# Optimization experiments

Hardware: AMD Instinct MI355X
Metric: run time of the kernel (lower is better)

The kernel has to match this reference:

```python
import jax, jax.numpy as jnp
import numpy as np

B, NN, F, H = 8, 1024, 256, 8
D = F // H
SCALE = D ** -0.5


def setup_inputs() -> dict:
    key = jax.random.key(0)
    ks = jax.random.split(key, 12)
    s = 0.02
    inp = {
        'ndata': jax.random.normal(ks[0], (B, NN, F), jnp.float32),
        'N': NN,
        'attn_bias': jax.random.normal(ks[1], (B, NN, NN, H), jnp.float32),
        'attn_mask': jax.random.randint(ks[2], (B, NN, NN), 0, 2).astype(bool),
        'Wq': jax.random.normal(ks[3], (F, F), jnp.float32) * s,
        'bq': jnp.zeros((F,), jnp.float32),
        'Wk': jax.random.normal(ks[4], (F, F), jnp.float32) * s,
        'bk': jnp.zeros((F,), jnp.float32),
        'Wv': jax.random.normal(ks[5], (F, F), jnp.float32) * s,
        'bv': jnp.zeros((F,), jnp.float32),
        'Wo': jax.random.normal(ks[6], (F, F), jnp.float32) * s,
        'bo': jnp.zeros((F,), jnp.float32),
    }
    return inp


def reference(ndata, N, attn_bias, attn_mask, Wq, bq, Wk, bk, Wv, bv, Wo, bo):
    b, n, f = ndata.shape
    # QKV projections (torch nn.Linear: x @ W.T + b), split heads
    q = (ndata @ Wq.T + bq).reshape(b, n, H, D) * SCALE
    k = (ndata @ Wk.T + bk).reshape(b, n, H, D)
    v = (ndata @ Wv.T + bv).reshape(b, n, H, D)
    # scores: (b, q, k, h) matching torch layout after its transposes
    scores = jnp.einsum('bqhd,bkhd->bqkh', q, k)
    scores = scores + attn_bias  # additive bias
    # original code force-unmasks column 0 so every row has a valid entry
    mask = attn_mask.at[:, :, 0].set(False)
    scores = jnp.where(mask[..., None], -jnp.inf, scores)
    attn = jax.nn.softmax(scores, axis=2)  # softmax over keys
    out = jnp.einsum('bqkh,bkhd->bqhd', attn, v).reshape(b, n, f)
    return out @ Wo.T + bo
```

## Files before the change

kernel.cpp:

```cpp
#include <hip/hip_runtime.h>
#include <hip/hip_bf16.h>

typedef __attribute__((ext_vector_type(8))) short short8;
typedef __attribute__((ext_vector_type(4))) float f32x4;

#define MFMA16(a,b,c) __builtin_amdgcn_mfma_f32_16x16x32_bf16((a),(b),(c),0,0,0)

static __device__ __forceinline__ unsigned int f2bf(float f){
    unsigned int u = __float_as_uint(f);
    u += 0x7FFFu + ((u >> 16) & 1u);
    return u >> 16;
}

static __device__ __forceinline__ short8 pack8(float4 a, float4 b){
    short8 r;
    r[0]=(short)f2bf(a.x); r[1]=(short)f2bf(a.y);
    r[2]=(short)f2bf(a.z); r[3]=(short)f2bf(a.w);
    r[4]=(short)f2bf(b.x); r[5]=(short)f2bf(b.y);
    r[6]=(short)f2bf(b.z); r[7]=(short)f2bf(b.w);
    return r;
}

__global__ __launch_bounds__(256) void mask_prep_k(
    const unsigned int* __restrict__ m, unsigned int* __restrict__ bmout)
{
    __shared__ int any_hi;
    const int tid  = threadIdx.x;
    const int lane = tid & 63;
    const unsigned int gbase = blockIdx.x*256u + tid;
    if (tid == 0) any_hi = 0;

    unsigned int wv[8]; unsigned int acc = 0;
    #pragma unroll
    for (int it = 0; it < 8; ++it){
        wv[it] = m[it*262144u + gbase];
        acc |= wv[it];
    }
    __syncthreads();
    if (acc & 0xFFFFFF00u) atomicOr(&any_hi, 1);
    __syncthreads();

    if (any_hi == 0){
        for (int it = 0; it < 32; ++it){
            unsigned int idx = it*262144u + gbase;
            unsigned int v = m[idx];
            unsigned long long bal = __ballot(v != 0u);
            if (lane == 0)
                *(unsigned long long*)(bmout + (idx >> 5)) = bal;
        }
    } else {
        #pragma unroll
        for (int it = 0; it < 8; ++it){
            unsigned int idx = it*262144u + gbase;
            unsigned int v = wv[it];
            unsigned int nib = (v | (v>>7) | (v>>14) | (v>>21)) & 0xFu;
            unsigned int x = nib << ((lane & 7)*4);
            x |= (unsigned int)__shfl_xor((int)x, 1);
            x |= (unsigned int)__shfl_xor((int)x, 2);
            x |= (unsigned int)__shfl_xor((int)x, 4);
            if ((lane & 7) == 0)
                bmout[idx >> 3] = x;
        }
    }
}

__global__ __launch_bounds__(256) void qkv_proj_k(
    const float* __restrict__ nd,
    const float* __restrict__ Wqp, const float* __restrict__ bqp,
    const float* __restrict__ Wkp, const float* __restrict__ bkp,
    const float* __restrict__ Wvp, const float* __restrict__ bvp,
    unsigned short* __restrict__ qout, unsigned short* __restrict__ kout,
    unsigned short* __restrict__ vtout)
{
    __shared__ __align__(16) unsigned short xl[64*264];
    const int tid  = threadIdx.x;
    const int bi   = blockIdx.x;
    const int kind = bi >> 7;
    const int R0   = (bi & 127) * 64;
    const int b    = R0 >> 10;
    const int n0   = R0 & 1023;

    #pragma unroll
    for (int it = 0; it < 16; ++it){
        int f4 = it*256 + tid;
        int r = f4 >> 6, c4 = f4 & 63;
        float4 v = *(const float4*)(nd + (size_t)(R0+r)*256 + c4*4);
        unsigned int lo = f2bf(v.x) | (f2bf(v.y) << 16);
        unsigned int hi = f2bf(v.z) | (f2bf(v.w) << 16);
        *(uint2*)&xl[r*264 + c4*4] = make_uint2(lo, hi);
    }
    __syncthreads();

    const int lane = tid & 63;
    const int w  = tid >> 6;
    const int ln = lane & 15;
    const int g  = lane >> 4;
    const int ow = w * 64;

    f32x4 acc[4][4];
    #pragma unroll
    for (int a=0;a<4;++a){
        #pragma unroll
        for (int c=0;c<4;++c) acc[a][c] = (f32x4){0.f,0.f,0.f,0.f};
    }

    if (kind < 2){
        const float* W  = kind ? Wkp : Wqp;
        const float* bb = kind ? bkp : bqp;
        unsigned short* op = kind ? kout : qout;
        const float scl = kind ? 1.0f : 0.17677669529663687f;
        for (int kk = 0; kk < 8; ++kk){
            short8 wf[4], xf[4];
            #pragma unroll
            for (int ot=0; ot<4; ++ot){
                const float* wp = W + (size_t)(ow + ot*16 + ln)*256 + kk*32 + g*8;
                wf[ot] = pack8(*(const float4*)wp, *(const float4*)(wp+4));
            }
            #pragma unroll
            for (int nt=0; nt<4; ++nt)
                xf[nt] = *(const short8*)&xl[(nt*16+ln)*264 + kk*32 + g*8];
            #pragma unroll
            for (int ot=0; ot<4; ++ot){
                #pragma unroll
                for (int nt=0; nt<4; ++nt)
                    acc[ot][nt] = MFMA16(wf[ot], xf[nt], acc[ot][nt]);
            }
        }
        #pragma unroll
        for (int ot=0; ot<4; ++ot){
            int o0 = ow + ot*16 + g*4;
            int h = o0 >> 5, d0 = o0 & 31;
            float4 b4 = *(const float4*)(bb + o0);
            #pragma unroll
            for (int nt=0; nt<4; ++nt){
                int n = n0 + nt*16 + ln;
                unsigned int lo = f2bf((acc[ot][nt][0]+b4.x)*scl) | (f2bf((acc[ot][nt][1]+b4.y)*scl)<<16);
                unsigned int hi = f2bf((acc[ot][nt][2]+b4.z)*scl) | (f2bf((acc[ot][nt][3]+b4.w)*scl)<<16);
                *(uint2*)(op + ((size_t)(b*8+h)*1024 + n)*32 + d0) = make_uint2(lo,hi);
            }
        }
    } else {
        for (int kk = 0; kk < 8; ++kk){
            short8 wf[4], xf[4];
            #pragma unroll
            for (int ot=0; ot<4; ++ot){
                const float* wp = Wvp + (size_t)(ow + ot*16 + ln)*256 + kk*32 + g*8;
                wf[ot] = pack8(*(const float4*)wp, *(const float4*)(wp+4));
            }
            #pragma unroll
            for (int nt=0; nt<4; ++nt)
                xf[nt] = *(const short8*)&xl[(nt*16+ln)*264 + kk*32 + g*8];
            #pragma unroll
            for (int nt=0; nt<4; ++nt){
                #pragma unroll
                for (int ot=0; ot<4; ++ot)
                    acc[nt][ot] = MFMA16(xf[nt], wf[ot], acc[nt][ot]);
            }
        }
        #pragma unroll
        for (int nt=0; nt<4; ++nt){
            int nb = n0 + nt*16 + g*4;
            #pragma unroll
            for (int ot=0; ot<4; ++ot){
                int o = ow + ot*16 + ln;
                int h = o >> 5, d = o & 31;
                float bvv = bvp[o];
                unsigned int lo = f2bf(acc[nt][ot][0]+bvv) | (f2bf(acc[nt][ot][1]+bvv)<<16);
                unsigned int hi = f2bf(acc[nt][ot][2]+bvv) | (f2bf(acc[nt][ot][3]+bvv)<<16);
                *(uint2*)(vtout + ((size_t)(b*8+h)*32 + d)*1024 + nb) = make_uint2(lo,hi);
            }
        }
    }
}

__global__ __launch_bounds__(512, 4) void attn_k(
    const unsigned short* __restrict__ qbuf, const unsigned short* __restrict__ kbuf,
    const unsigned short* __restrict__ vtbuf, const float* __restrict__ bias,
    const unsigned int* __restrict__ bm, unsigned short* __restrict__ ab)
{
    __shared__ __align__(16) float bs[8704];
    const int tid  = threadIdx.x;
    const int bi   = blockIdx.x;
    const int b    = bi >> 6;
    const int q0   = (bi & 63) * 16;
    const int lane = tid & 63;
    const int w    = tid >> 6;
    const int ln   = lane & 15;
    const int g    = lane >> 4;

    const short8 qf = *(const short8*)(qbuf + ((size_t)(b*8+w)*1024 + q0 + ln)*32 + g*8);

    const int kperm = ((ln >> 2) << 3) + (ln & 3);
    const unsigned short* kp = kbuf  + ((size_t)(b*8+w)*1024 + kperm)*32 + g*8;
    const unsigned short* vp = vtbuf + ((size_t)(b*8+w)*32   + ln)*1024 + g*8;
    const unsigned int*  bmp = bm + (size_t)(b*1024 + q0 + ln)*32;

    const int sq  = tid >> 5;
    const float* bgp = bias + (size_t)(b*1024 + q0 + sq)*8192 + (tid & 31)*4;
    const int hqb = (tid & 1)*4*1088 + sq*68;
    const int kpw = (tid & 31) >> 1;
    const int rb0 = w*1088 + ln*68 + 8*g;

    f32x4 acc0 = (f32x4){0.f,0.f,0.f,0.f};
    f32x4 acc1 = (f32x4){0.f,0.f,0.f,0.f};
    float lsum = 0.f;
    const f32x4 z4 = {0.f,0.f,0.f,0.f};

    float4 br0, br1, br2, br3;
    short8 kn0, kn1, kn2, kn3;
    unsigned int bm0, bm1;

#define LOAD_ALL(cc) do { int c_ = (cc); \
    br0 = *(const float4*)(bgp + (size_t)c_*512); \
    br1 = *(const float4*)(bgp + (size_t)c_*512 + 128); \
    br2 = *(const float4*)(bgp + (size_t)c_*512 + 256); \
    br3 = *(const float4*)(bgp + (size_t)c_*512 + 384); \
    kn0 = *(const short8*)(kp + c_*2048); \
    kn1 = *(const short8*)(kp + c_*2048 + 128); \
    kn2 = *(const short8*)(kp + c_*2048 + 1024); \
    kn3 = *(const short8*)(kp + c_*2048 + 1152); \
    bm0 = bmp[2*c_]; bm1 = bmp[2*c_+1]; } while(0)

#define STAGE1(R, IT) do { int kw_ = (IT)*16 + kpw; \
    bs[hqb        + kw_] = R.x; \
    bs[hqb + 1088 + kw_] = R.y; \
    bs[hqb + 2176 + kw_] = R.z; \
    bs[hqb + 3264 + kw_] = R.w; } while(0)

#define CHUNK_HALF(K0, K1, BMW, KH, VOFF) do { \
    f32x4 s0 = MFMA16(K0, qf, z4);    \
    f32x4 s1 = MFMA16(K1, qf, z4);    \
    f32x4 blo = *(const f32x4*)&bs[rb0 + (KH)*32]; \
    f32x4 bhi = *(const f32x4*)&bs[rb0 + (KH)*32 + 4]; \
    short8 vf0 = *(const short8*)(vp + (VOFF)); \
    short8 vf1 = *(const short8*)(vp + (VOFF) + 16*1024); \
    unsigned int mb_ = (BMW) >> (g*8); \
    float e0 = __expf(s0[0] + blo[0]); e0 = ((mb_>>0)&1u) ? 0.f : e0; \
    float e1 = __expf(s0[1] + blo[1]); e1 = ((mb_>>1)&1u) ? 0.f : e1; \
    float e2 = __expf(s0[2] + blo[2]); e2 = ((mb_>>2)&1u) ? 0.f : e2; \
    float e3 = __expf(s0[3] + blo[3]); e3 = ((mb_>>3)&1u) ? 0.f : e3; \
    float e4 = __expf(s1[0] + bhi[0]); e4 = ((mb_>>4)&1u) ? 0.f : e4; \
    float e5 = __expf(s1[1] + bhi[1]); e5 = ((mb_>>5)&1u) ? 0.f : e5; \
    float e6 = __expf(s1[2] + bhi[2]); e6 = ((mb_>>6)&1u) ? 0.f : e6; \
    float e7 = __expf(s1[3] + bhi[3]); e7 = ((mb_>>7)&1u) ? 0.f : e7; \
    lsum += ((e0+e1)+(e2+e3)) + ((e4+e5)+(e6+e7)); \
    int4 pw_ = make_int4( \
        (int)(f2bf(e0) | (f2bf(e1)<<16)), (int)(f2bf(e2) | (f2bf(e3)<<16)), \
        (int)(f2bf(e4) | (f2bf(e5)<<16)), (int)(f2bf(e6) | (f2bf(e7)<<16))); \
    short8 pf_ = *(short8*)&pw_; \
    acc0 = MFMA16(vf0, pf_, acc0); \
    acc1 = MFMA16(vf1, pf_, acc1); } while(0)

    LOAD_ALL(0);
    bm0 &= ~1u;

    #pragma unroll 1
    for (int cc = 0; cc < 16; ++cc){
        STAGE1(br0, 0); STAGE1(br1, 1); STAGE1(br2, 2); STAGE1(br3, 3);
        short8 ck0 = kn0, ck1 = kn1, ck2 = kn2, ck3 = kn3;
        unsigned int cb0 = bm0, cb1 = bm1;
        __syncthreads();
        if (cc + 1 < 16) LOAD_ALL(cc + 1);

        CHUNK_HALF(ck0, ck1, cb0, 0, cc*64);
        CHUNK_HALF(ck2, ck3, cb1, 1, cc*64 + 32);
        __syncthreads();
    }

    float ps = lsum;
    ps += __shfl_xor(ps, 16);
    ps += __shfl_xor(ps, 32);
    float inv = 1.0f / ps;
    {
        int n = q0 + ln;
        unsigned int lo0 = f2bf(acc0[0]*inv) | (f2bf(acc0[1]*inv)<<16);
        unsigned int hi0 = f2bf(acc0[2]*inv) | (f2bf(acc0[3]*inv)<<16);
        *(uint2*)(ab + ((size_t)(b*1024 + n))*256 + w*32 + g*4) = make_uint2(lo0,hi0);
        unsigned int lo1 = f2bf(acc1[0]*inv) | (f2bf(acc1[1]*inv)<<16);
        unsigned int hi1 = f2bf(acc1[2]*inv) | (f2bf(acc1[3]*inv)<<16);
        *(uint2*)(ab + ((size_t)(b*1024 + n))*256 + w*32 + 16 + g*4) = make_uint2(lo1,hi1);
    }
#undef LOAD_ALL
#undef STAGE1
#undef CHUNK_HALF
}

__global__ __launch_bounds__(256) void oproj_k(
    const unsigned short* __restrict__ ab, const float* __restrict__ Wop,
    const float* __restrict__ bop, float* __restrict__ out)
{
    __shared__ __align__(16) unsigned short al[32*264];
    const int tid = threadIdx.x;
    const int R0 = blockIdx.x * 32;
    #pragma unroll
    for (int it=0; it<4; ++it){
        int f8 = it*256 + tid;
        int r = f8 >> 5, c8 = f8 & 31;
        *(short8*)&al[r*264 + c8*8] = *(const short8*)(ab + (size_t)(R0+r)*256 + c8*8);
    }
    __syncthreads();
    const int lane = tid & 63;
    const int w = tid >> 6, ln = lane & 15, g = lane >> 4;
    const int ow = w*64;
    f32x4 acc[4][2];
    #pragma unroll
    for (int a=0;a<4;++a){ acc[a][0]=(f32x4){0.f,0.f,0.f,0.f}; acc[a][1]=(f32x4){0.f,0.f,0.f,0.f}; }
    for (int kk=0;kk<8;++kk){
        short8 wf[4], xf[2];
        #pragma unroll
        for (int ot=0;ot<4;++ot){
            const float* wp = Wop + (size_t)(ow+ot*16+ln)*256 + kk*32 + g*8;
            wf[ot] = pack8(*(const float4*)wp, *(const float4*)(wp+4));
        }
        #pragma unroll
        for (int nt=0;nt<2;++nt)
            xf[nt] = *(const short8*)&al[(nt*16+ln)*264 + kk*32 + g*8];
        #pragma unroll
        for (int ot=0;ot<4;++ot){
            #pragma unroll
            for (int nt=0;nt<2;++nt)
                acc[ot][nt] = MFMA16(wf[ot], xf[nt], acc[ot][nt]);
        }
    }
    #pragma unroll
    for (int ot=0;ot<4;++ot){
        int o0 = ow + ot*16 + g*4;
        float4 b4 = *(const float4*)(bop + o0);
        #pragma unroll
        for (int nt=0;nt<2;++nt){
            int n = R0 + nt*16 + ln;
            float4 res;
            res.x = acc[ot][nt][0] + b4.x;
            res.y = acc[ot][nt][1] + b4.y;
            res.z = acc[ot][nt][2] + b4.z;
            res.w = acc[ot][nt][3] + b4.w;
            *(float4*)(out + (size_t)n*256 + o0) = res;
        }
    }
}

extern "C" void kernel_launch(void* const* d_in, const int* in_sizes, int n_in,
                              void* d_out, int out_size, void* d_ws, size_t ws_size,
                              hipStream_t stream)
{
    (void)in_sizes; (void)n_in; (void)out_size; (void)ws_size;
    const float* nd   = (const float*)d_in[0];
    const float* bias = (const float*)d_in[2];
    const int* mask   = (const int*)d_in[3];
    const float* Wq = (const float*)d_in[4];
    const float* bq = (const float*)d_in[5];
    const float* Wk = (const float*)d_in[6];
    const float* bk = (const float*)d_in[7];
    const float* Wv = (const float*)d_in[8];
    const float* bv = (const float*)d_in[9];
    const float* Wo = (const float*)d_in[10];
    const float* bo = (const float*)d_in[11];
    float* out = (float*)d_out;

    const size_t ELEMS = (size_t)8*8*1024*32;
    unsigned short* qb  = (unsigned short*)d_ws;
    unsigned short* kb  = qb  + ELEMS;
    unsigned short* vtb = kb  + ELEMS;
    unsigned short* ab  = vtb + ELEMS;
    unsigned int* bmw   = (unsigned int*)(ab + ELEMS);

    mask_prep_k<<<1024, 256, 0, stream>>>((const unsigned int*)mask, bmw);
    qkv_proj_k<<<384, 256, 0, stream>>>(nd, Wq, bq, Wk, bk, Wv, bv, qb, kb, vtb);
    attn_k<<<512, 512, 0, stream>>>(qb, kb, vtb, bias, bmw, ab);
    oproj_k<<<256, 256, 0, stream>>>(ab, Wo, bo, out);
}
```

Before: 144.2 us.

## Split attention heads across two blocks of four waves each

The attention kernel now launches 1024 blocks of 256 threads, each handling four heads for a 16-query tile, instead of 512 blocks of 512 threads covering all eight heads. The shared bias staging buffer is halved and the bias loads are re-indexed so each block reads only its half of the head dimension (16-byte chunks at stride 32 bytes). The prefetch of the next chunk is also moved ahead of the barrier. The aim is more, smaller blocks for better occupancy and load balance, at the cost of less contiguous bias reads and the mask words being loaded twice.

```diff
diff --git a/kernel.cpp b/kernel.cpp
--- a/kernel.cpp
+++ b/kernel.cpp
@@ -173,32 +173,34 @@
     }
 }
 
-__global__ __launch_bounds__(512, 4) void attn_k(
+__global__ __launch_bounds__(256, 4) void attn_k(
     const unsigned short* __restrict__ qbuf, const unsigned short* __restrict__ kbuf,
     const unsigned short* __restrict__ vtbuf, const float* __restrict__ bias,
     const unsigned int* __restrict__ bm, unsigned short* __restrict__ ab)
 {
-    __shared__ __align__(16) float bs[8704];
+    __shared__ __align__(16) float bs[4352];
     const int tid  = threadIdx.x;
     const int bi   = blockIdx.x;
-    const int b    = bi >> 6;
+    const int hh   = bi >> 9;
+    const int b    = (bi >> 6) & 7;
     const int q0   = (bi & 63) * 16;
     const int lane = tid & 63;
     const int w    = tid >> 6;
     const int ln   = lane & 15;
     const int g    = lane >> 4;
-
-    const short8 qf = *(const short8*)(qbuf + ((size_t)(b*8+w)*1024 + q0 + ln)*32 + g*8);
+    const int h    = hh*4 + w;
+
+    const short8 qf = *(const short8*)(qbuf + ((size_t)(b*8+h)*1024 + q0 + ln)*32 + g*8);
 
     const int kperm = ((ln >> 2) << 3) + (ln & 3);
-    const unsigned short* kp = kbuf  + ((size_t)(b*8+w)*1024 + kperm)*32 + g*8;
-    const unsigned short* vp = vtbuf + ((size_t)(b*8+w)*32   + ln)*1024 + g*8;
+    const unsigned short* kp = kbuf  + ((size_t)(b*8+h)*1024 + kperm)*32 + g*8;
+    const unsigned short* vp = vtbuf + ((size_t)(b*8+h)*32   + ln)*1024 + g*8;
     const unsigned int*  bmp = bm + (size_t)(b*1024 + q0 + ln)*32;
 
-    const int sq  = tid >> 5;
-    const float* bgp = bias + (size_t)(b*1024 + q0 + sq)*8192 + (tid & 31)*4;
-    const int hqb = (tid & 1)*4*1088 + sq*68;
-    const int kpw = (tid & 31) >> 1;
+    const int sq  = tid >> 4;
+    const int sk  = tid & 15;
+    const float* bgp = bias + (size_t)(b*1024 + q0 + sq)*8192 + sk*8 + hh*4;
+    const int hqb = sq*68;
     const int rb0 = w*1088 + ln*68 + 8*g;
 
     f32x4 acc0 = (f32x4){0.f,0.f,0.f,0.f};
@@ -221,11 +223,11 @@
     kn3 = *(const short8*)(kp + c_*2048 + 1152); \
     bm0 = bmp[2*c_]; bm1 = bmp[2*c_+1]; } while(0)
 
-#define STAGE1(R, IT) do { int kw_ = (IT)*16 + kpw; \
-    bs[hqb        + kw_] = R.x; \
-    bs[hqb + 1088 + kw_] = R.y; \
-    bs[hqb + 2176 + kw_] = R.z; \
-    bs[hqb + 3264 + kw_] = R.w; } while(0)
+#define STAGE1(R, IT) do { int kw_ = hqb + (IT)*16 + sk; \
+    bs[kw_       ] = R.x; \
+    bs[kw_ + 1088] = R.y; \
+    bs[kw_ + 2176] = R.z; \
+    bs[kw_ + 3264] = R.w; } while(0)
 
 #define CHUNK_HALF(K0, K1, BMW, KH, VOFF) do { \
     f32x4 s0 = MFMA16(K0, qf, z4);    \
@@ -259,8 +261,8 @@
         STAGE1(br0, 0); STAGE1(br1, 1); STAGE1(br2, 2); STAGE1(br3, 3);
         short8 ck0 = kn0, ck1 = kn1, ck2 = kn2, ck3 = kn3;
         unsigned int cb0 = bm0, cb1 = bm1;
+        if (cc + 1 < 16) LOAD_ALL(cc + 1);
         __syncthreads();
-        if (cc + 1 < 16) LOAD_ALL(cc + 1);
 
         CHUNK_HALF(ck0, ck1, cb0, 0, cc*64);
         CHUNK_HALF(ck2, ck3, cb1, 1, cc*64 + 32);
@@ -275,10 +277,10 @@
         int n = q0 + ln;
         unsigned int lo0 = f2bf(acc0[0]*inv) | (f2bf(acc0[1]*inv)<<16);
         unsigned int hi0 = f2bf(acc0[2]*inv) | (f2bf(acc0[3]*inv)<<16);
-        *(uint2*)(ab + ((size_t)(b*1024 + n))*256 + w*32 + g*4) = make_uint2(lo0,hi0);
+        *(uint2*)(ab + ((size_t)(b*1024 + n))*256 + h*32 + g*4) = make_uint2(lo0,hi0);
         unsigned int lo1 = f2bf(acc1[0]*inv) | (f2bf(acc1[1]*inv)<<16);
         unsigned int hi1 = f2bf(acc1[2]*inv) | (f2bf(acc1[3]*inv)<<16);
-        *(uint2*)(ab + ((size_t)(b*1024 + n))*256 + w*32 + 16 + g*4) = make_uint2(lo1,hi1);
+        *(uint2*)(ab + ((size_t)(b*1024 + n))*256 + h*32 + 16 + g*4) = make_uint2(lo1,hi1);
     }
 #undef LOAD_ALL
 #undef STAGE1
@@ -366,6 +368,6 @@
 
     mask_prep_k<<<1024, 256, 0, stream>>>((const unsigned int*)mask, bmw);
     qkv_proj_k<<<384, 256, 0, stream>>>(nd, Wq, bq, Wk, bk, Wv, bv, qb, kb, vtb);
-    attn_k<<<512, 512, 0, stream>>>(qb, kb, vtb, bias, bmw, ab);
+    attn_k<<<1024, 256, 0, stream>>>(qb, kb, vtb, bias, bmw, ab);
     oproj_k<<<256, 256, 0, stream>>>(ab, Wo, bo, out);
 }
```

Result: slower. 163.3 us (+13.3%).

## Merge mask prep into QKV kernel, stream bias with nontemporal loads, hoist prefetch

Applied to the files above, without the earlier changes.

Folds the mask bit-packing kernel into the QKV projection launch as extra blocks, so the two independent jobs run concurrently and one launch is saved. The streamed attention-bias and mask reads switch to nontemporal loads to reduce cache pollution. The next-chunk prefetch is moved ahead of the barrier so global loads are issued earlier. Risks include higher register pressure in the attention loop and the shared-memory footprint of the merged kernel limiting occupancy for the mask blocks.

```diff
diff --git a/kernel.cpp b/kernel.cpp
--- a/kernel.cpp
+++ b/kernel.cpp
@@ -21,59 +21,57 @@
     return r;
 }
 
-__global__ __launch_bounds__(256) void mask_prep_k(
-    const unsigned int* __restrict__ m, unsigned int* __restrict__ bmout)
-{
-    __shared__ int any_hi;
-    const int tid  = threadIdx.x;
-    const int lane = tid & 63;
-    const unsigned int gbase = blockIdx.x*256u + tid;
-    if (tid == 0) any_hi = 0;
-
-    unsigned int wv[8]; unsigned int acc = 0;
-    #pragma unroll
-    for (int it = 0; it < 8; ++it){
-        wv[it] = m[it*262144u + gbase];
-        acc |= wv[it];
-    }
-    __syncthreads();
-    if (acc & 0xFFFFFF00u) atomicOr(&any_hi, 1);
-    __syncthreads();
-
-    if (any_hi == 0){
-        for (int it = 0; it < 32; ++it){
-            unsigned int idx = it*262144u + gbase;
-            unsigned int v = m[idx];
-            unsigned long long bal = __ballot(v != 0u);
-            if (lane == 0)
-                *(unsigned long long*)(bmout + (idx >> 5)) = bal;
-        }
-    } else {
-        #pragma unroll
-        for (int it = 0; it < 8; ++it){
-            unsigned int idx = it*262144u + gbase;
-            unsigned int v = wv[it];
-            unsigned int nib = (v | (v>>7) | (v>>14) | (v>>21)) & 0xFu;
-            unsigned int x = nib << ((lane & 7)*4);
-            x |= (unsigned int)__shfl_xor((int)x, 1);
-            x |= (unsigned int)__shfl_xor((int)x, 2);
-            x |= (unsigned int)__shfl_xor((int)x, 4);
-            if ((lane & 7) == 0)
-                bmout[idx >> 3] = x;
-        }
-    }
-}
-
-__global__ __launch_bounds__(256) void qkv_proj_k(
+__global__ __launch_bounds__(256) void qkv_mask_k(
     const float* __restrict__ nd,
     const float* __restrict__ Wqp, const float* __restrict__ bqp,
     const float* __restrict__ Wkp, const float* __restrict__ bkp,
     const float* __restrict__ Wvp, const float* __restrict__ bvp,
     unsigned short* __restrict__ qout, unsigned short* __restrict__ kout,
-    unsigned short* __restrict__ vtout)
+    unsigned short* __restrict__ vtout,
+    const unsigned int* __restrict__ m, unsigned int* __restrict__ bmout)
 {
     __shared__ __align__(16) unsigned short xl[64*264];
     const int tid  = threadIdx.x;
+
+    if (blockIdx.x >= 384){
+        __shared__ int any_hi;
+        const int lane = tid & 63;
+        const unsigned int gbase = (blockIdx.x - 384)*256u + tid;
+        if (tid == 0) any_hi = 0;
+        unsigned int wv[8]; unsigned int acc = 0;
+        #pragma unroll
+        for (int it = 0; it < 8; ++it){
+            wv[it] = __builtin_nontemporal_load(m + it*262144u + gbase);
+            acc |= wv[it];
+        }
+        __syncthreads();
+        if (acc & 0xFFFFFF00u) atomicOr(&any_hi, 1);
+        __syncthreads();
+        if (any_hi == 0){
+            for (int it = 0; it < 32; ++it){
+                unsigned int idx = it*262144u + gbase;
+                unsigned int v = __builtin_nontemporal_load(m + idx);
+                unsigned long long bal = __ballot(v != 0u);
+                if (lane == 0)
+                    *(unsigned long long*)(bmout + (idx >> 5)) = bal;
+            }
+        } else {
+            #pragma unroll
+            for (int it = 0; it < 8; ++it){
+                unsigned int idx = it*262144u + gbase;
+                unsigned int v = wv[it];
+                unsigned int nib = (v | (v>>7) | (v>>14) | (v>>21)) & 0xFu;
+                unsigned int x = nib << ((lane & 7)*4);
+                x |= (unsigned int)__shfl_xor((int)x, 1);
+                x |= (unsigned int)__shfl_xor((int)x, 2);
+                x |= (unsigned int)__shfl_xor((int)x, 4);
+                if ((lane & 7) == 0)
+                    bmout[idx >> 3] = x;
+            }
+        }
+        return;
+    }
+
     const int bi   = blockIdx.x;
     const int kind = bi >> 7;
     const int R0   = (bi & 127) * 64;
@@ -206,15 +204,15 @@
     float lsum = 0.f;
     const f32x4 z4 = {0.f,0.f,0.f,0.f};
 
-    float4 br0, br1, br2, br3;
+    f32x4 br0, br1, br2, br3;
     short8 kn0, kn1, kn2, kn3;
     unsigned int bm0, bm1;
 
 #define LOAD_ALL(cc) do { int c_ = (cc); \
-    br0 = *(const float4*)(bgp + (size_t)c_*512); \
-    br1 = *(const float4*)(bgp + (size_t)c_*512 + 128); \
-    br2 = *(const float4*)(bgp + (size_t)c_*512 + 256); \
-    br3 = *(const float4*)(bgp + (size_t)c_*512 + 384); \
+    br0 = __builtin_nontemporal_load((const f32x4*)(bgp + (size_t)c_*512)); \
+    br1 = __builtin_nontemporal_load((const f32x4*)(bgp + (size_t)c_*512 + 128)); \
+    br2 = __builtin_nontemporal_load((const f32x4*)(bgp + (size_t)c_*512 + 256)); \
+    br3 = __builtin_nontemporal_load((const f32x4*)(bgp + (size_t)c_*512 + 384)); \
     kn0 = *(const short8*)(kp + c_*2048); \
     kn1 = *(const short8*)(kp + c_*2048 + 128); \
     kn2 = *(const short8*)(kp + c_*2048 + 1024); \
@@ -222,10 +220,10 @@
     bm0 = bmp[2*c_]; bm1 = bmp[2*c_+1]; } while(0)
 
 #define STAGE1(R, IT) do { int kw_ = (IT)*16 + kpw; \
-    bs[hqb        + kw_] = R.x; \
-    bs[hqb + 1088 + kw_] = R.y; \
-    bs[hqb + 2176 + kw_] = R.z; \
-    bs[hqb + 3264 + kw_] = R.w; } while(0)
+    bs[hqb        + kw_] = R[0]; \
+    bs[hqb + 1088 + kw_] = R[1]; \
+    bs[hqb + 2176 + kw_] = R[2]; \
+    bs[hqb + 3264 + kw_] = R[3]; } while(0)
 
 #define CHUNK_HALF(K0, K1, BMW, KH, VOFF) do { \
     f32x4 s0 = MFMA16(K0, qf, z4);    \
@@ -259,8 +257,8 @@
         STAGE1(br0, 0); STAGE1(br1, 1); STAGE1(br2, 2); STAGE1(br3, 3);
         short8 ck0 = kn0, ck1 = kn1, ck2 = kn2, ck3 = kn3;
         unsigned int cb0 = bm0, cb1 = bm1;
+        if (cc + 1 < 16) LOAD_ALL(cc + 1);
         __syncthreads();
-        if (cc + 1 < 16) LOAD_ALL(cc + 1);
 
         CHUNK_HALF(ck0, ck1, cb0, 0, cc*64);
         CHUNK_HALF(ck2, ck3, cb1, 1, cc*64 + 32);
@@ -364,8 +362,9 @@
     unsigned short* ab  = vtb + ELEMS;
     unsigned int* bmw   = (unsigned int*)(ab + ELEMS);
 
-    mask_prep_k<<<1024, 256, 0, stream>>>((const unsigned int*)mask, bmw);
-    qkv_proj_k<<<384, 256, 0, stream>>>(nd, Wq, bq, Wk, bk, Wv, bv, qb, kb, vtb);
+    qkv_mask_k<<<1408, 256, 0, stream>>>(nd, Wq, bq, Wk, bk, Wv, bv,
+                                         qb, kb, vtb,
+                                         (const unsigned int*)mask, bmw);
     attn_k<<<512, 512, 0, stream>>>(qb, kb, vtb, bias, bmw, ab);
     oproj_k<<<256, 256, 0, stream>>>(ab, Wo, bo, out);
 }
```

Result: faster. 137.3 us (-4.8%).
